# Kernel tuning notes

Measured on AMD Instinct MI355X. Metric: run time of the kernel, lower is better.

The kernel has to match this reference:

```python
import jax, jax.numpy as jnp
import numpy as np

PHI = (1.0 + 5.0 ** 0.5) / 2.0
TWO_PI = 2.0 * np.pi
LN_EPS = 1e-5


def _complex_linear(xr, xi, Wr, Wi, br, bi):
    # (Wr + i*Wi) @ (xr + i*xi) + (br + i*bi)
    yr = xr @ Wr.T - xi @ Wi.T + br
    yi = xr @ Wi.T + xi @ Wr.T + bi
    return yr, yi


def _layernorm(x, g, b):
    m = jnp.mean(x, axis=-1, keepdims=True)
    v = jnp.mean((x - m) ** 2, axis=-1, keepdims=True)
    return (x - m) * jax.lax.rsqrt(v + LN_EPS) * g + b


def reference(w, b, ip_Wr, ip_Wi, ip_br, ip_bi, ln_g, ln_b, W_qkv, log_alpha, op_Wr, op_Wi):
    B, S, D = w.shape
    H = log_alpha.shape[0]
    Dh = D // H
    scale = jnp.sqrt(jnp.asarray(Dh, w.dtype))
    alpha = jax.nn.sigmoid(log_alpha)[None, :, None]  # (1,H,1)
    ts = jnp.arange(S, dtype=w.dtype)

    def step(carry, xs):
        hr, hi, vs = carry          # (B,D),(B,D),(B,H,Dh)
        w_t, b_t, t = xs            # (B,D),(B,D),()
        # InstrumentedEulerTransform: separated theta, complex product
        wl = 1.0 + jnp.abs(w_t)
        tphi = (t * PHI) % TWO_PI   # wrap_time_periodic
        thr = hr / wl + b_t + tphi
        thi = hi / wl + b_t + tphi
        sr, cr = jnp.sin(thr), jnp.cos(thr)
        si, ci = jnp.sin(thi), jnp.cos(thi)
        hr2 = cr * ci - sr * si
        hi2 = cr * si + sr * ci
        # InstrumentedEchoChamber.forward_step
        pr, pi_ = _complex_linear(hr2, hi2, ip_Wr, ip_Wi, ip_br, ip_bi)
        xc = _layernorm(pr + pi_, ln_g, ln_b)
        qkv = (xc @ W_qkv.T).reshape(B, 3, H, Dh)
        q, k, v = qkv[:, 0], qkv[:, 1], qkv[:, 2]
        vs2 = alpha * v + (1.0 - alpha) * vs
        gate = jax.nn.sigmoid(jnp.sum(q * k, axis=-1, keepdims=True) / scale)
        retr = (gate * vs2).reshape(B, D)
        # output_proj ComplexLinear on (retr, 0), no bias
        ore = retr @ op_Wr.T
        oim = retr @ op_Wi.T
        return (hr2, hi2, vs2), (ore, oim)

    init = (jnp.zeros((B, D), w.dtype), jnp.zeros((B, D), w.dtype),
            jnp.zeros((B, H, Dh), w.dtype))
    wT = jnp.swapaxes(w, 0, 1)  # (S,B,D)
    bT = jnp.swapaxes(b, 0, 1)
    _, (or_seq, oi_seq) = jax.lax.scan(step, init, (wT, bT, ts))
    out = jnp.stack([or_seq, oi_seq])      # (2,S,B,D)
    return jnp.swapaxes(out, 1, 2)         # (2,B,S,D)


def setup_inputs() -> dict:
    key = jax.random.key(0)
    ks = jax.random.split(key, 10)
    B, S, D, H = 8, 2048, 512, 8
    s = 0.02
    return {
        "w": jax.random.normal(ks[0], (B, S, D), jnp.float32),
        "b": jax.random.normal(ks[1], (B, S, D), jnp.float32),
        "ip_Wr": jax.random.normal(ks[2], (D, D), jnp.float32) * s,
        "ip_Wi": jax.random.normal(ks[3], (D, D), jnp.float32) * s,
        "ip_br": jax.random.normal(ks[4], (D,), jnp.float32) * s,
        "ip_bi": jax.random.normal(ks[5], (D,), jnp.float32) * s,
        "ln_g": jnp.ones((D,), jnp.float32),
        "ln_b": jnp.zeros((D,), jnp.float32),
        "W_qkv": jax.random.normal(ks[6], (3 * D, D), jnp.float32) * s,
        "log_alpha": jax.random.normal(ks[7], (H,), jnp.float32),
        "op_Wr": jax.random.normal(ks[8], (D, D), jnp.float32) * s,
        "op_Wi": jax.random.normal(ks[9], (D, D), jnp.float32) * s,
    }
```

## Files before the change

### kernel.cpp

```cpp
#include <hip/hip_runtime.h>
#include <math.h>

#define BB 8
#define SS 2048
#define DD 512
#define HH 8
#define MM (BB*SS)

#define CHK 128
#define CL  16
#define CW  48

#define RT 32
#define RW 128

typedef unsigned short u16;
typedef unsigned int   u32;
typedef float f32x4 __attribute__((ext_vector_type(4)));
typedef short s16x8 __attribute__((ext_vector_type(8)));

__device__ __forceinline__ u16 f2bf(float x){
  union { float f; unsigned u; } c; c.f = x;
  unsigned r = c.u + 0x7FFF + ((c.u >> 16) & 1);
  return (u16)(r >> 16);
}
__device__ __forceinline__ float bf2f(u16 x){
  union { unsigned u; float f; } c; c.u = ((unsigned)x) << 16;
  return c.f;
}
__device__ __forceinline__ void gload16(const u16* g, u16* l){
  __builtin_amdgcn_global_load_lds(
      (const __attribute__((address_space(1))) unsigned int*)g,
      (__attribute__((address_space(3))) unsigned int*)l, 16, 0, 0);
}

__global__ void prep_all(const float* __restrict__ ipWr, const float* __restrict__ ipWi,
                         const float* __restrict__ Wqkv,
                         const float* __restrict__ opWr, const float* __restrict__ opWi,
                         const float* __restrict__ ipbr, const float* __restrict__ ipbi,
                         const float* __restrict__ la,
                         u16* __restrict__ W1, u16* __restrict__ Wq, u16* __restrict__ W3,
                         float* __restrict__ tphi2, float* __restrict__ bc,
                         float* __restrict__ alph){
  int id = blockIdx.x*256 + threadIdx.x;
  if (id < 524288){
    int n = id >> 10, k = id & 1023;
    int d = k >> 1;
    float v = (k & 1) ? (ipWr[n*512+d] - ipWi[n*512+d])
                      : (ipWr[n*512+d] + ipWi[n*512+d]);
    W1[id] = f2bf(v);
  } else if (id < 1310720){
    int i = id - 524288;
    Wq[i] = f2bf(Wqkv[i]);
  } else if (id < 1835008){
    int i = id - 1310720;
    int n = i >> 9, k = i & 511;
    W3[i] = f2bf((n < 512) ? opWr[n*512+k] : opWi[(n-512)*512+k]);
  } else if (id < 1837056){
    int t = id - 1835008;
    const float PHI_F    = 1.61803398874989484820f;
    const float TWO_PI_F = 6.28318530717958647693f;
    tphi2[t] = 2.0f * fmodf((float)t * PHI_F, TWO_PI_F);
  } else if (id < 1837568){
    int t = id - 1837056;
    bc[t] = ipbr[t] + ipbi[t];
  } else if (id < 1837576){
    int t = id - 1837568;
    alph[t] = 1.0f/(1.0f + expf(-la[t]));
  }
}

__global__ __launch_bounds__(256) void scan_h(const float* __restrict__ w,
                                              const float* __restrict__ bb,
                                              const float* __restrict__ tphi2,
                                              u32* __restrict__ X32){
  const int e = blockIdx.x*256 + threadIdx.x;
  const int c = blockIdx.y;
  const int b = e >> 9;
  const int d = e & 511;
  const float SQRT2 = 1.41421356237309504880f;
  const float PI_4  = 0.78539816339744830962f;
  const int tstart = c*CL;
  int t0 = tstart - CW; if (t0 < 0) t0 = 0;
  const int nw = tstart - t0;

  const float* wp = w  + ((size_t)b*SS + t0)*DD + d;
  const float* bp = bb + ((size_t)b*SS + t0)*DD + d;
  const float* tp = tphi2 + t0;

  const int U = 8;
  float wv[U], bv[U], wn[U], bn[U];

  float ss = 0.f;
  const int ngw = nw >> 3;
  if (ngw > 0){
    #pragma unroll
    for (int i=0;i<U;i++){ wv[i] = wp[(size_t)i*DD]; bv[i] = bp[(size_t)i*DD]; }
    for (int gg=0; gg<ngw; ++gg){
      if (gg+1 < ngw){
        const float* wnp = wp + (size_t)(gg+1)*U*DD;
        const float* bnp = bp + (size_t)(gg+1)*U*DD;
        #pragma unroll
        for (int i=0;i<U;i++){ wn[i] = wnp[(size_t)i*DD]; bn[i] = bnp[(size_t)i*DD]; }
      }
      #pragma unroll
      for (int i=0;i<U;i++){
        float rwl2 = SQRT2 * __builtin_amdgcn_rcpf(1.0f + fabsf(wv[i]));
        float cw   = fmaf(2.0f, bv[i], tp[gg*U+i]) + PI_4;
        ss = __sinf(fmaf(ss, rwl2, cw));
      }
      #pragma unroll
      for (int i=0;i<U;i++){ wv[i]=wn[i]; bv[i]=bn[i]; }
    }
  }
  float hs = SQRT2 * ss;

  const float* wq = wp + (size_t)nw*DD;
  const float* bq = bp + (size_t)nw*DD;
  const float* tq = tp + nw;
  u32* xp = X32 + (size_t)(b*SS + tstart)*512 + d;

  #pragma unroll
  for (int i=0;i<U;i++){ wv[i] = wq[(size_t)i*DD]; bv[i] = bq[(size_t)i*DD]; }
  for (int gg=0; gg<CL/U; ++gg){
    if (gg+1 < CL/U){
      const float* wnp = wq + (size_t)(gg+1)*U*DD;
      const float* bnp = bq + (size_t)(gg+1)*U*DD;
      #pragma unroll
      for (int i=0;i<U;i++){ wn[i] = wnp[(size_t)i*DD]; bn[i] = bnp[(size_t)i*DD]; }
    }
    #pragma unroll
    for (int i=0;i<U;i++){
      float rwl = __builtin_amdgcn_rcpf(1.0f + fabsf(wv[i]));
      float cc  = fmaf(2.0f, bv[i], tq[gg*U+i]);
      float theta = fmaf(hs, rwl, cc);
      float sn = __sinf(theta);
      float cs = __cosf(theta);
      hs = cs + sn;
      xp[(size_t)(gg*U+i)*512] = (u32)f2bf(cs) | ((u32)f2bf(sn) << 16);
    }
    #pragma unroll
    for (int i=0;i<U;i++){ wv[i]=wn[i]; bv[i]=bn[i]; }
  }
}

template<int TAG, int EPI>
__global__ __launch_bounds__(512) void gemm_bf16(const u16* __restrict__ A,
                                                 const u16* __restrict__ W,
                                                 float* __restrict__ C0,
                                                 float* __restrict__ C1,
                                                 u16* __restrict__ C2,
                                                 int N, int K){
  __shared__ __align__(16) u16 As[4][128*32];
  __shared__ __align__(16) u16 Bs[4][256*32];
  const int tid  = threadIdx.x;
  const int nwgx = gridDim.x;
  const int nwg  = nwgx * gridDim.y;
  const int lin  = blockIdx.y * nwgx + blockIdx.x;
  const int qq   = nwg >> 3;
  const int logi = (lin & 7) * qq + (lin >> 3);
  const int m0   = (logi / nwgx) * 128;
  const int n0   = (logi % nwgx) * 256;

  const int wave = tid >> 6;
  const int lane = tid & 63;
  const int wm   = wave >> 2;
  const int wn   = wave & 3;
  const int l15  = lane & 15;
  const int g    = lane >> 4;

  const int kgs  = (tid & 3) ^ ((tid >> 3) & 3);
  const u16* Asrc  = A + (size_t)(m0 + (tid>>2)) * K + kgs*8;
  const u16* Bsrc0 = W + (size_t)(n0 + (tid>>2)) * K + kgs*8;
  const u16* Bsrc1 = Bsrc0 + (size_t)128 * K;
  const int dA  = tid*8;
  const int dB0 = tid*8;
  const int dB1 = tid*8 + 4096;

  f32x4 acc[4][4];
  #pragma unroll
  for (int i=0;i<4;i++)
    #pragma unroll
    for (int j=0;j<4;j++) acc[i][j] = (f32x4){0.f,0.f,0.f,0.f};

#define STAGE(reg, koff) do {                  \
    gload16(Asrc  + (koff), &As[reg][dA]);     \
    gload16(Bsrc0 + (koff), &Bs[reg][dB0]);    \
    gload16(Bsrc1 + (koff), &Bs[reg][dB1]);    \
  } while(0)

  const int H = K >> 5;
  STAGE(0, 0);
  STAGE(1, 32);
  STAGE(2, 64);
  asm volatile("s_waitcnt vmcnt(6)" ::: "memory");
  __builtin_amdgcn_s_barrier();

  for (int h = 0; h < H; ++h){
    const u16* Ah = &As[h & 3][0];
    const u16* Bh = &Bs[h & 3][0];
    s16x8 af[4], bf[4];
    #pragma unroll
    for (int s=0;s<4;s++){
      int rA = wm*64 + s*16 + l15;
      af[s] = *(const s16x8*)&Ah[rA*32 + ((g ^ ((rA>>1)&3))*8)];
      int rB = wn*64 + s*16 + l15;
      bf[s] = *(const s16x8*)&Bh[rB*32 + ((g ^ ((rB>>1)&3))*8)];
    }
    if (h + 3 < H) STAGE((h+3) & 3, (h+3)*32);
    __builtin_amdgcn_s_barrier();
    __builtin_amdgcn_s_setprio(1);
    #pragma unroll
    for (int mi=0;mi<4;mi++)
      #pragma unroll
      for (int ni=0;ni<4;ni++)
        acc[mi][ni] = __builtin_amdgcn_mfma_f32_16x16x32_bf16(af[mi], bf[ni], acc[mi][ni], 0, 0, 0);
    __builtin_amdgcn_s_setprio(0);
    int rem = H - 1 - h;
    if      (rem >= 3) asm volatile("s_waitcnt vmcnt(6)" ::: "memory");
    else if (rem == 2) asm volatile("s_waitcnt vmcnt(3)" ::: "memory");
    else if (rem == 1) asm volatile("s_waitcnt vmcnt(0)" ::: "memory");
    __builtin_amdgcn_s_barrier();
  }

#undef STAGE

  #pragma unroll
  for (int mi=0;mi<4;mi++){
    #pragma unroll
    for (int j=0;j<4;j++){
      int r = m0 + wm*64 + mi*16 + g*4 + j;
      #pragma unroll
      for (int ni=0;ni<4;ni++){
        int col = n0 + wn*64 + ni*16 + l15;
        float v = acc[mi][ni][j];
        if (EPI == 1){
          if (col < 512) C0[(size_t)r*512 + col]       = v;
          else           C1[(size_t)r*512 + (col-512)] = v;
        } else {
          C2[(size_t)r*N + col] = f2bf(v);
        }
      }
    }
  }
}

__global__ __launch_bounds__(256) void ln_kernel(const u16* __restrict__ y,
                                                 const float* __restrict__ bc,
                                                 const float* __restrict__ g,
                                                 const float* __restrict__ bb,
                                                 u16* __restrict__ xc){
  const int row  = blockIdx.x*4 + (threadIdx.x >> 6);
  const int lane = threadIdx.x & 63;
  s16x8 v = *(const s16x8*)(y + (size_t)row*512 + lane*8);
  float4 c0 = ((const float4*)bc)[lane*2];
  float4 c1 = ((const float4*)bc)[lane*2+1];
  float f[8];
  f[0] = bf2f((u16)v[0]) + c0.x; f[1] = bf2f((u16)v[1]) + c0.y;
  f[2] = bf2f((u16)v[2]) + c0.z; f[3] = bf2f((u16)v[3]) + c0.w;
  f[4] = bf2f((u16)v[4]) + c1.x; f[5] = bf2f((u16)v[5]) + c1.y;
  f[6] = bf2f((u16)v[6]) + c1.z; f[7] = bf2f((u16)v[7]) + c1.w;
  float s = 0.f, s2 = 0.f;
  #pragma unroll
  for (int i=0;i<8;i++){ s += f[i]; s2 = fmaf(f[i], f[i], s2); }
  #pragma unroll
  for (int off=32; off>0; off>>=1){ s += __shfl_xor(s, off); s2 += __shfl_xor(s2, off); }
  float mean = s * (1.0f/512.0f);
  float var  = s2 * (1.0f/512.0f) - mean*mean;
  float rstd = rsqrtf(var + 1e-5f);
  float4 g0 = ((const float4*)g)[lane*2],  g1 = ((const float4*)g)[lane*2+1];
  float4 b0 = ((const float4*)bb)[lane*2], b1 = ((const float4*)bb)[lane*2+1];
  s16x8 o;
  o[0] = (short)f2bf((f[0]-mean)*rstd*g0.x + b0.x);
  o[1] = (short)f2bf((f[1]-mean)*rstd*g0.y + b0.y);
  o[2] = (short)f2bf((f[2]-mean)*rstd*g0.z + b0.z);
  o[3] = (short)f2bf((f[3]-mean)*rstd*g0.w + b0.w);
  o[4] = (short)f2bf((f[4]-mean)*rstd*g1.x + b1.x);
  o[5] = (short)f2bf((f[5]-mean)*rstd*g1.y + b1.y);
  o[6] = (short)f2bf((f[6]-mean)*rstd*g1.z + b1.z);
  o[7] = (short)f2bf((f[7]-mean)*rstd*g1.w + b1.w);
  *(s16x8*)(xc + (size_t)row*512 + lane*8) = o;
}

__global__ __launch_bounds__(256) void retr_fused(const u16* __restrict__ qkv,
                                                  const float* __restrict__ alph,
                                                  u16* __restrict__ retr){
  const int wid  = blockIdx.x*4 + (threadIdx.x >> 6);
  const int lane = threadIdx.x & 63;
  const int c = wid & 63;
  const int h = (wid >> 6) & 7;
  const int b = wid >> 9;
  const float a  = alph[h];
  const float om = 1.0f - a;
  const int d  = h*64 + lane;
  const int t0 = c*RT;
  int w0 = t0 - RW; if (w0 < 0) w0 = 0;
  const int nw = t0 - w0;

  const u16* vp = qkv + ((size_t)(b*SS + w0))*1536 + 1024 + d;
  float vs = 0.f;
  {
    const int U = 8;
    float vv[U], vn[U];
    const int ng = nw >> 3;
    if (ng > 0){
      #pragma unroll
      for (int i=0;i<U;i++) vv[i] = bf2f(vp[(size_t)i*1536]);
      for (int gg=0; gg<ng; ++gg){
        if (gg+1 < ng){
          const u16* vnp = vp + (size_t)(gg+1)*U*1536;
          #pragma unroll
          for (int i=0;i<U;i++) vn[i] = bf2f(vnp[(size_t)i*1536]);
        }
        #pragma unroll
        for (int i=0;i<U;i++) vs = fmaf(a, vv[i], om*vs);
        #pragma unroll
        for (int i=0;i<U;i++) vv[i] = vn[i];
      }
    }
  }
  const u16* qp = qkv + ((size_t)(b*SS + t0))*1536 + d;
  u16* op = retr + ((size_t)(b*SS + t0))*512 + d;
  #pragma unroll 4
  for (int i=0;i<RT;i++){
    float q  = bf2f(qp[(size_t)i*1536]);
    float kk = bf2f(qp[(size_t)i*1536 + 512]);
    float v  = bf2f(qp[(size_t)i*1536 + 1024]);
    vs = fmaf(a, v, om*vs);
    float p = q*kk;
    #pragma unroll
    for (int off=32; off>0; off>>=1) p += __shfl_xor(p, off);
    float gate = 1.0f/(1.0f + __expf(-p*0.125f));
    op[(size_t)i*512] = f2bf(gate * vs);
  }
}

extern "C" void kernel_launch(void* const* d_in, const int* in_sizes, int n_in,
                              void* d_out, int out_size, void* d_ws, size_t ws_size,
                              hipStream_t stream) {
  const float* w    = (const float*)d_in[0];
  const float* b    = (const float*)d_in[1];
  const float* ipWr = (const float*)d_in[2];
  const float* ipWi = (const float*)d_in[3];
  const float* ipbr = (const float*)d_in[4];
  const float* ipbi = (const float*)d_in[5];
  const float* lng  = (const float*)d_in[6];
  const float* lnb  = (const float*)d_in[7];
  const float* Wqkv = (const float*)d_in[8];
  const float* la   = (const float*)d_in[9];
  const float* opWr = (const float*)d_in[10];
  const float* opWi = (const float*)d_in[11];
  float* out0 = (float*)d_out;
  float* out1 = out0 + (size_t)MM*DD;

  char* base = (char*)d_ws;
  u16*   W1    = (u16*)  (base + 0);
  u16*   Wq    = (u16*)  (base + 1048576);
  u16*   W3    = (u16*)  (base + 2621440);
  float* bc    = (float*)(base + 3670016);
  float* alph  = (float*)(base + 3672064);
  float* tphi2 = (float*)(base + 3672128);
  u32*   X32   = (u32*)  (base + 3680384);
  u16*   y     = (u16*)  (base + 37234816);
  u16*   xc    = (u16*)  (base + 54012032);
  u16*   qkv   = (u16*)  (base + 70789248);
  u16*   retr  = (u16*)X32;

  prep_all<<<7179,256,0,stream>>>(ipWr, ipWi, Wqkv, opWr, opWi, ipbr, ipbi, la,
                                  W1, Wq, W3, tphi2, bc, alph);

  scan_h<<<dim3(16,CHK),256,0,stream>>>(w, b, tphi2, X32);

  gemm_bf16<1,2><<<dim3(2,128),512,0,stream>>>((const u16*)X32, W1, nullptr, nullptr, y, 512, 1024);
  ln_kernel<<<4096,256,0,stream>>>(y, bc, lng, lnb, xc);
  gemm_bf16<2,2><<<dim3(6,128),512,0,stream>>>(xc, Wq, nullptr, nullptr, qkv, 1536, 512);

  retr_fused<<<1024,256,0,stream>>>(qkv, alph, retr);

  gemm_bf16<3,1><<<dim3(4,128),512,0,stream>>>(retr, W3, out0, out1, nullptr, 1024, 512);
}
```

Before: 163.2 us.

## Load GEMM B fragments directly from global into registers, enlarge retr chunk

The GEMM kernel no longer stages the weight (B) tile through LDS. Each wave now loads its B fragments straight from global memory into registers, double-buffered across k-steps, while only the A tile keeps the LDS ring. The vmcnt waits and barriers are adjusted to match. Separately, retr_fused processes 64-step chunks instead of 32, halving its grid, which cuts redundant warm-up window work but also reduces parallelism.

Measured after the change: 228.6 us. 40.1% more time.

```diff
diff --git a/kernel.cpp b/kernel.cpp
--- a/kernel.cpp
+++ b/kernel.cpp
@@ -11,7 +11,7 @@
 #define CL  16
 #define CW  48
 
-#define RT 32
+#define RT 64
 #define RW 128
 
 typedef unsigned short u16;
@@ -152,7 +152,6 @@
                                                  u16* __restrict__ C2,
                                                  int N, int K){
   __shared__ __align__(16) u16 As[4][128*32];
-  __shared__ __align__(16) u16 Bs[4][256*32];
   const int tid  = threadIdx.x;
   const int nwgx = gridDim.x;
   const int nwg  = nwgx * gridDim.y;
@@ -169,13 +168,10 @@
   const int l15  = lane & 15;
   const int g    = lane >> 4;
 
-  const int kgs  = (tid & 3) ^ ((tid >> 3) & 3);
-  const u16* Asrc  = A + (size_t)(m0 + (tid>>2)) * K + kgs*8;
-  const u16* Bsrc0 = W + (size_t)(n0 + (tid>>2)) * K + kgs*8;
-  const u16* Bsrc1 = Bsrc0 + (size_t)128 * K;
-  const int dA  = tid*8;
-  const int dB0 = tid*8;
-  const int dB1 = tid*8 + 4096;
+  const int kgs = (tid & 3) ^ ((tid >> 3) & 3);
+  const u16* Asrc = A + (size_t)(m0 + (tid>>2)) * K + kgs*8;
+  const int dA = tid*8;
+  const u16* Bf = W + (size_t)(n0 + wn*64 + l15) * K + g*8;
 
   f32x4 acc[4][4];
   #pragma unroll
@@ -183,47 +179,55 @@
     #pragma unroll
     for (int j=0;j<4;j++) acc[i][j] = (f32x4){0.f,0.f,0.f,0.f};
 
-#define STAGE(reg, koff) do {                  \
-    gload16(Asrc  + (koff), &As[reg][dA]);     \
-    gload16(Bsrc0 + (koff), &Bs[reg][dB0]);    \
-    gload16(Bsrc1 + (koff), &Bs[reg][dB1]);    \
+  const int H = K >> 5;
+  s16x8 b0[4], b1[4];
+
+#define PHASE(hh, bcur, bnxt) do {                                        \
+    const u16* Ah = &As[(hh)&3][0];                                       \
+    s16x8 af[4];                                                          \
+    _Pragma("unroll")                                                     \
+    for (int s=0;s<4;s++){                                                \
+      int rA = wm*64 + s*16 + l15;                                        \
+      af[s] = *(const s16x8*)&Ah[rA*32 + ((g ^ ((rA>>1)&3))*8)];          \
+    }                                                                     \
+    if ((hh)+1 < H){                                                      \
+      _Pragma("unroll")                                                   \
+      for (int s=0;s<4;s++)                                               \
+        bnxt[s] = *(const s16x8*)(Bf + (size_t)s*16*K + ((hh)+1)*32);     \
+    }                                                                     \
+    if ((hh)+3 < H)                                                       \
+      gload16(Asrc + ((hh)+3)*32, &As[((hh)+3)&3][dA]);                   \
+    __builtin_amdgcn_s_barrier();                                         \
+    __builtin_amdgcn_s_setprio(1);                                        \
+    _Pragma("unroll")                                                     \
+    for (int mi=0;mi<4;mi++)                                              \
+      _Pragma("unroll")                                                   \
+      for (int ni=0;ni<4;ni++)                                            \
+        acc[mi][ni] = __builtin_amdgcn_mfma_f32_16x16x32_bf16(af[mi], bcur[ni], acc[mi][ni], 0, 0, 0); \
+    __builtin_amdgcn_s_setprio(0);                                        \
+    {                                                                     \
+      int rem = H - 1 - (hh);                                             \
+      if      (rem >= 3) asm volatile("s_waitcnt vmcnt(6)" ::: "memory"); \
+      else if (rem == 2) asm volatile("s_waitcnt vmcnt(5)" ::: "memory"); \
+      else if (rem == 1) asm volatile("s_waitcnt vmcnt(4)" ::: "memory"); \
+      if (rem > 0) __builtin_amdgcn_s_barrier();                          \
+    }                                                                     \
   } while(0)
 
-  const int H = K >> 5;
-  STAGE(0, 0);
-  STAGE(1, 32);
-  STAGE(2, 64);
-  asm volatile("s_waitcnt vmcnt(6)" ::: "memory");
+  #pragma unroll
+  for (int s=0;s<4;s++) b0[s] = *(const s16x8*)(Bf + (size_t)s*16*K);
+  gload16(Asrc,      &As[0][dA]);
+  gload16(Asrc + 32, &As[1][dA]);
+  gload16(Asrc + 64, &As[2][dA]);
+  asm volatile("s_waitcnt vmcnt(2)" ::: "memory");
   __builtin_amdgcn_s_barrier();
 
-  for (int h = 0; h < H; ++h){
-    const u16* Ah = &As[h & 3][0];
-    const u16* Bh = &Bs[h & 3][0];
-    s16x8 af[4], bf[4];
-    #pragma unroll
-    for (int s=0;s<4;s++){
-      int rA = wm*64 + s*16 + l15;
-      af[s] = *(const s16x8*)&Ah[rA*32 + ((g ^ ((rA>>1)&3))*8)];
-      int rB = wn*64 + s*16 + l15;
-      bf[s] = *(const s16x8*)&Bh[rB*32 + ((g ^ ((rB>>1)&3))*8)];
-    }
-    if (h + 3 < H) STAGE((h+3) & 3, (h+3)*32);
-    __builtin_amdgcn_s_barrier();
-    __builtin_amdgcn_s_setprio(1);
-    #pragma unroll
-    for (int mi=0;mi<4;mi++)
-      #pragma unroll
-      for (int ni=0;ni<4;ni++)
-        acc[mi][ni] = __builtin_amdgcn_mfma_f32_16x16x32_bf16(af[mi], bf[ni], acc[mi][ni], 0, 0, 0);
-    __builtin_amdgcn_s_setprio(0);
-    int rem = H - 1 - h;
-    if      (rem >= 3) asm volatile("s_waitcnt vmcnt(6)" ::: "memory");
-    else if (rem == 2) asm volatile("s_waitcnt vmcnt(3)" ::: "memory");
-    else if (rem == 1) asm volatile("s_waitcnt vmcnt(0)" ::: "memory");
-    __builtin_amdgcn_s_barrier();
-  }
-
-#undef STAGE
+  for (int h = 0; h < H; h += 2){
+    PHASE(h,   b0, b1);
+    PHASE(h+1, b1, b0);
+  }
+
+#undef PHASE
 
   #pragma unroll
   for (int mi=0;mi<4;mi++){
@@ -287,9 +291,9 @@
                                                   u16* __restrict__ retr){
   const int wid  = blockIdx.x*4 + (threadIdx.x >> 6);
   const int lane = threadIdx.x & 63;
-  const int c = wid & 63;
-  const int h = (wid >> 6) & 7;
-  const int b = wid >> 9;
+  const int c = wid & 31;
+  const int h = (wid >> 5) & 7;
+  const int b = wid >> 8;
   const float a  = alph[h];
   const float om = 1.0f - a;
   const int d  = h*64 + lane;
@@ -375,7 +379,7 @@
   ln_kernel<<<4096,256,0,stream>>>(y, bc, lng, lnb, xc);
   gemm_bf16<2,2><<<dim3(6,128),512,0,stream>>>(xc, Wq, nullptr, nullptr, qkv, 1536, 512);
 
-  retr_fused<<<1024,256,0,stream>>>(qkv, alph, retr);
+  retr_fused<<<512,256,0,stream>>>(qkv, alph, retr);
 
   gemm_bf16<3,1><<<dim3(4,128),512,0,stream>>>(retr, W3, out0, out1, nullptr, 1024, 512);
 }
```
